# Kernel optimization log

Measured on AMD Instinct MI355X. Metric: run time of the kernel, lower is better.

Reference implementation:

```python
import jax, jax.numpy as jnp
import numpy as np

NUM_NEURONS = 256
NUM_SAMPLES = 512
MAX_SPIKES = 32
N_STEPS = 32          # fixed RK4 steps per spike round (stands in for adaptive Tsit5)
ALPHA = 0.03
V_RESET = 1.0
T0 = 0.0


def setup_inputs() -> dict:
    key = jax.random.key(0)
    ks = jax.random.split(key, 7)
    input_current = jax.random.normal(ks[0], (NUM_NEURONS,), dtype=jnp.float32)
    # _build_w with network=all-False: uniform(minval=0.5), mask sets nothing
    w = jax.random.uniform(ks[1], (NUM_NEURONS, NUM_NEURONS), minval=0.5, maxval=1.0, dtype=jnp.float32)
    mu = jax.random.uniform(ks[2], (2,), minval=0.5, maxval=1.0, dtype=jnp.float32)
    v0 = jax.random.normal(ks[3], (NUM_NEURONS,), dtype=jnp.float32)
    i0 = jax.random.normal(ks[4], (NUM_NEURONS,), dtype=jnp.float32)
    # s0 = log(U) - alpha  (always < 0)
    s0 = (jnp.log(jax.random.uniform(ks[5], (NUM_SAMPLES, NUM_NEURONS), minval=1e-6, maxval=1.0)) - ALPHA).astype(jnp.float32)
    # pre-drawn stochastic resets, one per (spike round, sample, neuron)
    reset_s = (jnp.log(jax.random.uniform(ks[6], (MAX_SPIKES, NUM_SAMPLES, NUM_NEURONS), minval=1e-6, maxval=1.0)) - ALPHA).astype(jnp.float32)
    return dict(input_current=input_current, w=w, mu=mu, v0=v0, i0=i0, s0=s0, reset_s=reset_s, t1=2)


def _drift(y, ic, mu1, mu2):
    # y: [samples, neurons, 3] = (v, i, s)
    v, i = y[..., 0], y[..., 1]
    dv = mu1 * (i + ic - v)
    di = -mu2 * i
    ds = jax.nn.sigmoid(v)  # intensity_fn(v)
    return jnp.stack([dv, di, ds], axis=-1)


def reference(input_current, w, mu, v0, i0, s0, reset_s, t1):
    t1f = jnp.float32(t1)
    mu1, mu2 = mu[0], mu[1]
    ic = input_current  # constant-in-time input current, [neurons]

    y0 = jnp.concatenate([
        jnp.broadcast_to(v0, (NUM_SAMPLES, NUM_NEURONS))[..., None],
        jnp.broadcast_to(i0, (NUM_SAMPLES, NUM_NEURONS))[..., None],
        s0[..., None]], axis=-1)  # [samples, neurons, 3]

    def rk4(y, h):
        k1 = _drift(y, ic, mu1, mu2)
        k2 = _drift(y + 0.5 * h * k1, ic, mu1, mu2)
        k3 = _drift(y + 0.5 * h * k2, ic, mu1, mu2)
        k4 = _drift(y + h * k3, ic, mu1, mu2)
        return y + (h / 6.0) * (k1 + 2.0 * k2 + 2.0 * k3 + k4)

    def round_body(carry, reset_k):
        t0s, y_in = carry                      # t0s: [samples]
        dt = (t1f - t0s) / N_STEPS             # per-sample step size
        h = dt[:, None, None]

        def step(sc, _):
            t, y, done, tev, yev, emask = sc
            y_new = rk4(y, h)
            y_new = jnp.where(done[:, None, None], y, y_new)  # freeze after event
            s_prev, s_new = y[..., 2], y_new[..., 2]
            crossed = s_new > 0.0                              # cond_fn root: s crosses 0
            trig = crossed.any(axis=1) & (~done)
            idx = jnp.argmax(s_new, axis=1)                    # event neuron (first/largest crossing)
            sp = jnp.take_along_axis(s_prev, idx[:, None], 1)[:, 0]
            sn = jnp.take_along_axis(s_new, idx[:, None], 1)[:, 0]
            frac = jnp.clip(sp / (sp - sn + 1e-12), 0.0, 1.0)  # linear root estimate (Newton stand-in)
            t_c = t + frac * dt
            y_c = y + frac[:, None, None] * (y_new - y)
            tev = jnp.where(trig, t_c, tev)
            yev = jnp.where(trig[:, None, None], y_c, yev)
            emask = jnp.where(trig[:, None], crossed, emask)
            y = jnp.where(trig[:, None, None], y_c, y_new)
            done = done | trig
            return (t + dt, y, done, tev, yev, emask), None

        done0 = jnp.zeros((NUM_SAMPLES,), bool)
        tev0 = jnp.full((NUM_SAMPLES,), jnp.inf, jnp.float32)
        em0 = jnp.zeros((NUM_SAMPLES, NUM_NEURONS), bool)
        (_, yend, done, tev, yev, emask), _ = jax.lax.scan(
            step, (t0s, y_in, done0, tev0, y_in, em0), None, length=N_STEPS)

        tev = jnp.where(done, tev, t1f)                 # no event -> sol.ts[-1] = t1
        yev = jnp.where(done[:, None, None], yev, yend)

        # trans_fn: spike reset + synaptic jump w[event_idx]
        eidx = jnp.argmax(emask, axis=1)
        w_row = jnp.where(done[:, None], w[eidx], 0.0)  # zero if no event happened
        v_t = yev[..., 0] - jnp.where(emask, V_RESET, 0.0)
        i_t = yev[..., 1] + w_row
        s_t = jnp.minimum(jnp.where(emask, reset_k, yev[..., 2]), 0.0)
        y_next = jnp.stack([v_t, i_t, s_t], axis=-1)
        return (tev, y_next), (tev, yev, emask)

    t0s = jnp.full((NUM_SAMPLES,), T0, jnp.float32)
    _, (tevs, yevs, emasks) = jax.lax.scan(jax.checkpoint(round_body), (t0s, y0), reset_s)

    spike_times = jnp.transpose(tevs, (1, 0))            # [samples, max_spikes]
    spike_values = jnp.transpose(yevs, (1, 0, 2, 3))     # [samples, max_spikes, neurons, 3]
    spike_marks = jnp.transpose(emasks, (1, 0, 2))       # [samples, max_spikes, neurons]
    return spike_times, spike_values, spike_marks
```

## Files before the change

### kernel.cpp

```cpp
#include <hip/hip_runtime.h>
#include <math.h>

#define NN 256
#define NS 512
#define MS 32
#define NSTEP 32
#define VRESET 1.0f

__device__ __forceinline__ float sigf(float x) {
    float e = __expf(-x);
    return __builtin_amdgcn_rcpf(1.0f + e);
}

__device__ __forceinline__ void block_sync_lds() {
    asm volatile("s_waitcnt lgkmcnt(0)" ::: "memory");
    __builtin_amdgcn_s_barrier();
    asm volatile("" ::: "memory");
}

__device__ __forceinline__ void rk4step(float v, float ii, float s,
                                        float ic, float mu1, float mu2,
                                        float dt, float hh, float h6,
                                        float& vn, float& in_, float& sn)
{
    float kv1 = mu1 * (ii + ic - v);
    float ki1 = -mu2 * ii;
    float ks1 = sigf(v);
    float v2 = v + hh * kv1;
    float i2 = ii + hh * ki1;
    float kv2 = mu1 * (i2 + ic - v2);
    float ki2 = -mu2 * i2;
    float ks2 = sigf(v2);
    float v3 = v + hh * kv2;
    float i3 = ii + hh * ki2;
    float kv3 = mu1 * (i3 + ic - v3);
    float ki3 = -mu2 * i3;
    float ks3 = sigf(v3);
    float v4 = v + dt * kv3;
    float i4 = ii + dt * ki3;
    float kv4 = mu1 * (i4 + ic - v4);
    float ki4 = -mu2 * i4;
    float ks4 = sigf(v4);
    vn  = v  + h6 * (kv1 + 2.0f * kv2 + 2.0f * kv3 + kv4);
    in_ = ii + h6 * (ki1 + 2.0f * ki2 + 2.0f * ki3 + ki4);
    sn  = s  + h6 * (ks1 + 2.0f * ks2 + 2.0f * ks3 + ks4);
}

__global__ __launch_bounds__(256) void snn_kernel(
    const float* __restrict__ ic_g,
    const float* __restrict__ w,
    const float* __restrict__ mu,
    const float* __restrict__ v0,
    const float* __restrict__ i0,
    const float* __restrict__ s0,
    const float* __restrict__ reset_s,
    const int*   __restrict__ t1p,
    float* __restrict__ out)
{
    const int tid  = threadIdx.x;
    const int lane = tid & 63;
    const int wid  = tid >> 6;
    const int samp = blockIdx.x;
    const float mu1 = mu[0];
    const float mu2 = mu[1];
    const float t1f = (float)t1p[0];

    __shared__ int4  s_any4[4];
    __shared__ float s_sn[NN];
    __shared__ float s_sp[NN];
    __shared__ unsigned long long s_key[4];
    __shared__ int   s_eidx[4];

    float v  = v0[tid];
    float ii = i0[tid];
    float s  = s0[samp * NN + tid];
    const float ic = ic_g[tid];
    float t0 = 0.0f;

    float* times = out;
    float* vals  = out + (size_t)NS * MS;
    float* marks = out + (size_t)NS * MS * (1 + NN * 3);

    for (int r = 0; r < MS; ++r) {
        const float rs = reset_s[((size_t)r * NS + samp) * NN + tid];

        const float dt = (t1f - t0) / (float)NSTEP;
        float tev = t1f;
        float yv = v, yi = ii, ys = s;
        bool  em = false;
        bool  done = false;
        float wr = 0.0f;

        if (dt != 0.0f) {
            const float hh = 0.5f * dt;
            const float h6 = dt * (1.0f / 6.0f);

            float pv = v, pi_ = ii, ps = s;
            float cv, ci, cs;
            rk4step(pv, pi_, ps, ic, mu1, mu2, dt, hh, h6, cv, ci, cs);
            float t = t0;

            for (int st = 0; st < NSTEP; ++st) {
                unsigned long long bl = __ballot(cs > 0.0f);
                if (lane == 0)
                    ((int*)&s_any4[st & 3])[wid] = (bl != 0ull) ? 1 : 0;

                float kv1 = mu1 * (ci + ic - cv);
                float ki1 = -mu2 * ci;
                float ks1 = sigf(cv);
                float v2 = cv + hh * kv1;
                float i2 = ci + hh * ki1;
                float kv2 = mu1 * (i2 + ic - v2);
                float ki2 = -mu2 * i2;
                float ks2 = sigf(v2);

                __builtin_amdgcn_sched_barrier(0);
                block_sync_lds();
                __builtin_amdgcn_sched_barrier(0);

                int4 f = s_any4[st & 3];

                float v3 = cv + hh * kv2;
                float i3 = ci + hh * ki2;
                float kv3 = mu1 * (i3 + ic - v3);
                float ki3 = -mu2 * i3;
                float ks3 = sigf(v3);
                float v4 = cv + dt * kv3;
                float i4 = ci + dt * ki3;
                float kv4 = mu1 * (i4 + ic - v4);
                float ki4 = -mu2 * i4;
                float ks4 = sigf(v4);
                float nv  = cv + h6 * (kv1 + 2.0f * kv2 + 2.0f * kv3 + kv4);
                float ni  = ci + h6 * (ki1 + 2.0f * ki2 + 2.0f * ki3 + ki4);
                float ns_ = cs + h6 * (ks1 + 2.0f * ks2 + 2.0f * ks3 + ks4);

                int af = f.x | f.y | f.z | f.w;

                if (af) {
                    bool crossed = cs > 0.0f;
                    s_sn[tid] = cs;
                    s_sp[tid] = ps;

                    unsigned int b = __float_as_uint(cs);
                    unsigned int m = (b & 0x80000000u) ? 0xFFFFFFFFu : 0x80000000u;
                    unsigned long long key =
                        ((unsigned long long)(b ^ m) << 32) |
                        (unsigned int)(NN - 1 - tid);
#pragma unroll
                    for (int off = 32; off >= 1; off >>= 1) {
                        unsigned long long o = __shfl_xor(key, off);
                        key = (o > key) ? o : key;
                    }
                    unsigned long long bm = __ballot(crossed);
                    int cand = (bm != 0ull)
                                   ? (wid * 64 + (int)__builtin_ctzll(bm))
                                   : (2 * NN);
                    if (lane == 0) { s_key[wid] = key; s_eidx[wid] = cand; }
                    block_sync_lds();

                    unsigned long long k0 = s_key[0], k1 = s_key[1];
                    unsigned long long k2 = s_key[2], k3 = s_key[3];
                    k0 = (k1 > k0) ? k1 : k0;
                    k2 = (k3 > k2) ? k3 : k2;
                    k0 = (k2 > k0) ? k2 : k0;
                    int bn = NN - 1 - (int)(unsigned int)(k0 & 0xFFFFFFFFull);

                    int eidx = s_eidx[0];
                    eidx = (s_eidx[1] < eidx) ? s_eidx[1] : eidx;
                    eidx = (s_eidx[2] < eidx) ? s_eidx[2] : eidx;
                    eidx = (s_eidx[3] < eidx) ? s_eidx[3] : eidx;

                    wr = w[eidx * NN + tid];

                    float bv  = s_sn[bn];
                    float bsp = s_sp[bn];
                    float frac = bsp / (bsp - bv + 1e-12f);
                    frac = fminf(fmaxf(frac, 0.0f), 1.0f);
                    tev = t + frac * dt;
                    yv = pv  + frac * (cv - pv);
                    yi = pi_ + frac * (ci - pi_);
                    ys = ps  + frac * (cs - ps);
                    em = crossed;
                    done = true;
                    break;
                }

                pv = cv; pi_ = ci; ps = cs;
                cv = nv; ci = ni; cs = ns_;
                t += dt;
            }

            if (!done) { yv = cv; yi = ci; ys = cs; }
        }

        const int sr = samp * MS + r;
        if (tid == 0) times[sr] = tev;
        {
            float* p = vals + ((size_t)sr * NN + tid) * 3;
            p[0] = yv;
            p[1] = yi;
            p[2] = ys;
            marks[(size_t)sr * NN + tid] = em ? 1.0f : 0.0f;
        }

        if (done) {
            v  = yv - (em ? VRESET : 0.0f);
            ii = yi + wr;
            float sres = em ? rs : ys;
            s = fminf(sres, 0.0f);
        } else {
            v = yv; ii = yi;
            s = fminf(ys, 0.0f);
        }
        t0 = tev;
    }
}

extern "C" void kernel_launch(void* const* d_in, const int* in_sizes, int n_in,
                              void* d_out, int out_size, void* d_ws, size_t ws_size,
                              hipStream_t stream) {
    const float* ic      = (const float*)d_in[0];
    const float* w       = (const float*)d_in[1];
    const float* mu      = (const float*)d_in[2];
    const float* v0      = (const float*)d_in[3];
    const float* i0      = (const float*)d_in[4];
    const float* s0      = (const float*)d_in[5];
    const float* reset_s = (const float*)d_in[6];
    const int*   t1p     = (const int*)d_in[7];
    float* out = (float*)d_out;

    snn_kernel<<<dim3(NS), dim3(256), 0, stream>>>(ic, w, mu, v0, i0, s0,
                                                   reset_s, t1p, out);
}
```

Baseline: 135.9 us.

## Drop second barrier in spike event detection by publishing state every step

Each thread now writes its current and previous s values to a double-buffered shared array on every RK4 step, and each wave's lane 0 stores the index of its first crossing neuron in the flag word. When an event is seen, every wave finds the max-s neuron across all 256 entries on its own, using float4 LDS reads and a 32-bit shuffle reduction. This removes the extra block barrier and the 64-bit key exchange from the event path. The cost is two LDS stores on every step, and the final no-event state handling changes so the loop stops advancing after its last step.

```diff
diff --git a/kernel.cpp b/kernel.cpp
--- a/kernel.cpp
+++ b/kernel.cpp
@@ -65,11 +65,9 @@
     const float mu2 = mu[1];
     const float t1f = (float)t1p[0];
 
-    __shared__ int4  s_any4[4];
-    __shared__ float s_sn[NN];
-    __shared__ float s_sp[NN];
-    __shared__ unsigned long long s_key[4];
-    __shared__ int   s_eidx[4];
+    __shared__ int4 s_flag[4];
+    __shared__ __align__(16) float s_sn[2][NN];
+    __shared__ __align__(16) float s_sp[2][NN];
 
     float v  = v0[tid];
     float ii = i0[tid];
@@ -82,6 +80,7 @@
     float* marks = out + (size_t)NS * MS * (1 + NN * 3);
 
     for (int r = 0; r < MS; ++r) {
+        const int buf = r & 1;
         const float rs = reset_s[((size_t)r * NS + samp) * NN + tid];
 
         const float dt = (t1f - t0) / (float)NSTEP;
@@ -101,9 +100,15 @@
             float t = t0;
 
             for (int st = 0; st < NSTEP; ++st) {
+                s_sn[buf][tid] = cs;
+                s_sp[buf][tid] = ps;
                 unsigned long long bl = __ballot(cs > 0.0f);
-                if (lane == 0)
-                    ((int*)&s_any4[st & 3])[wid] = (bl != 0ull) ? 1 : 0;
+                if (lane == 0) {
+                    int meta = (bl != 0ull)
+                        ? ((((wid << 6) + (int)__builtin_ctzll(bl)) << 1) | 1)
+                        : 0;
+                    ((int*)&s_flag[st & 3])[wid] = meta;
+                }
 
                 float kv1 = mu1 * (ci + ic - cv);
                 float ki1 = -mu2 * ci;
@@ -118,7 +123,7 @@
                 block_sync_lds();
                 __builtin_amdgcn_sched_barrier(0);
 
-                int4 f = s_any4[st & 3];
+                int4 f = s_flag[st & 3];
 
                 float v3 = cv + hh * kv2;
                 float i3 = ci + hh * ki2;
@@ -134,60 +139,59 @@
                 float ni  = ci + h6 * (ki1 + 2.0f * ki2 + 2.0f * ki3 + ki4);
                 float ns_ = cs + h6 * (ks1 + 2.0f * ks2 + 2.0f * ks3 + ks4);
 
-                int af = f.x | f.y | f.z | f.w;
-
-                if (af) {
-                    bool crossed = cs > 0.0f;
-                    s_sn[tid] = cs;
-                    s_sp[tid] = ps;
-
-                    unsigned int b = __float_as_uint(cs);
-                    unsigned int m = (b & 0x80000000u) ? 0xFFFFFFFFu : 0x80000000u;
-                    unsigned long long key =
-                        ((unsigned long long)(b ^ m) << 32) |
-                        (unsigned int)(NN - 1 - tid);
+                if ((f.x | f.y | f.z | f.w) & 1) {
+                    const float4 q =
+                        *(const float4*)&s_sn[buf][lane << 2];
+                    int e0 = (f.x & 1) ? (f.x >> 1) : (2 * NN);
+                    int e1 = (f.y & 1) ? (f.y >> 1) : (2 * NN);
+                    int e2 = (f.z & 1) ? (f.z >> 1) : (2 * NN);
+                    int e3 = (f.w & 1) ? (f.w >> 1) : (2 * NN);
+                    int ea = e0 < e1 ? e0 : e1;
+                    int eb = e2 < e3 ? e2 : e3;
+                    int eidx = ea < eb ? ea : eb;
+                    wr = w[eidx * NN + tid];
+
+                    unsigned bx = __float_as_uint(q.x);
+                    unsigned by = __float_as_uint(q.y);
+                    unsigned bz = __float_as_uint(q.z);
+                    unsigned bw = __float_as_uint(q.w);
+                    unsigned k0 = (bx & 0x80000000u) ? ~bx : (bx | 0x80000000u);
+                    unsigned k1 = (by & 0x80000000u) ? ~by : (by | 0x80000000u);
+                    unsigned k2 = (bz & 0x80000000u) ? ~bz : (bz | 0x80000000u);
+                    unsigned k3 = (bw & 0x80000000u) ? ~bw : (bw | 0x80000000u);
+                    unsigned km = k0; int pos = 0;
+                    if (k1 > km) { km = k1; pos = 1; }
+                    if (k2 > km) { km = k2; pos = 2; }
+                    if (k3 > km) { km = k3; pos = 3; }
+                    unsigned red = km;
 #pragma unroll
                     for (int off = 32; off >= 1; off >>= 1) {
-                        unsigned long long o = __shfl_xor(key, off);
-                        key = (o > key) ? o : key;
+                        unsigned o = __shfl_xor(red, off);
+                        red = (o > red) ? o : red;
                     }
-                    unsigned long long bm = __ballot(crossed);
-                    int cand = (bm != 0ull)
-                                   ? (wid * 64 + (int)__builtin_ctzll(bm))
-                                   : (2 * NN);
-                    if (lane == 0) { s_key[wid] = key; s_eidx[wid] = cand; }
-                    block_sync_lds();
-
-                    unsigned long long k0 = s_key[0], k1 = s_key[1];
-                    unsigned long long k2 = s_key[2], k3 = s_key[3];
-                    k0 = (k1 > k0) ? k1 : k0;
-                    k2 = (k3 > k2) ? k3 : k2;
-                    k0 = (k2 > k0) ? k2 : k0;
-                    int bn = NN - 1 - (int)(unsigned int)(k0 & 0xFFFFFFFFull);
-
-                    int eidx = s_eidx[0];
-                    eidx = (s_eidx[1] < eidx) ? s_eidx[1] : eidx;
-                    eidx = (s_eidx[2] < eidx) ? s_eidx[2] : eidx;
-                    eidx = (s_eidx[3] < eidx) ? s_eidx[3] : eidx;
-
-                    wr = w[eidx * NN + tid];
-
-                    float bv  = s_sn[bn];
-                    float bsp = s_sp[bn];
+                    unsigned long long cm = __ballot(km == red);
+                    int L = (int)__builtin_ctzll(cm);
+                    int wpos = __builtin_amdgcn_readlane(pos, L);
+                    int bn = (L << 2) + wpos;
+
+                    float bv  = s_sn[buf][bn];
+                    float bsp = s_sp[buf][bn];
                     float frac = bsp / (bsp - bv + 1e-12f);
                     frac = fminf(fmaxf(frac, 0.0f), 1.0f);
                     tev = t + frac * dt;
                     yv = pv  + frac * (cv - pv);
                     yi = pi_ + frac * (ci - pi_);
                     ys = ps  + frac * (cs - ps);
-                    em = crossed;
+                    em = (cs > 0.0f);
                     done = true;
                     break;
                 }
 
-                pv = cv; pi_ = ci; ps = cs;
-                cv = nv; ci = ni; cs = ns_;
-                t += dt;
+                if (st + 1 < NSTEP) {
+                    pv = cv; pi_ = ci; ps = cs;
+                    cv = nv; ci = ni; cs = ns_;
+                    t += dt;
+                }
             }
 
             if (!done) { yv = cv; yi = ci; ys = cs; }
```

Measured after the change: 132.9 us. 1.02x faster.
